# Performance work log

Measured on AMD Instinct MI355X. Metric: run time of the kernel, lower is better.

## Reference

```python
import jax, jax.numpy as jnp
import numpy as np

B, L = 8, 512
D_MODEL, N_HEAD, N_GLOBAL, N_ITER = 64, 8, 64, 4
DAMP_H = 0.0; DAMP_Z = 0.0; STEP_H = 1.0; STEP_Z = 1.0; REG_H = 1.0; REG_Z = 1.0
NEG = -1e9; BIG = 1e9


def sin_pe(length, d):
    # standard additive sinusoidal positional encoding (AddPositionalEncoding)
    pos = np.arange(length, dtype=np.float32)[:, None]
    div = np.exp(np.arange(0, d, 2, dtype=np.float32) * (-np.log(10000.0) / d))
    pe = np.zeros((length, d), dtype=np.float32)
    pe[:, 0::2] = np.sin(pos * div)
    pe[:, 1::2] = np.cos(pos * div)
    return jnp.asarray(pe)


def setup_inputs() -> dict:
    key = jax.random.key(0)
    k1, k2, k3 = jax.random.split(key, 3)
    x = jax.random.normal(k1, (B, L, D_MODEL), jnp.float32)
    mask = jnp.ones((B, L), jnp.int32)
    ternary = jax.random.normal(k2, (D_MODEL, D_MODEL, N_HEAD), jnp.float32)  # std=1 init
    global_w = jax.random.normal(k3, (N_GLOBAL, D_MODEL, 1), jnp.float32) / np.sqrt(D_MODEL)
    return {"x": x, "mask": mask, "ternary": ternary, "global_w": global_w}


def _forward(x, mask, ternary, global_w):
    Bq, Lq, d = x.shape
    norm = lambda a: jax.nn.softmax(a, axis=-1)
    valid = (mask != 0)
    m1 = valid[:, :, None].astype(x.dtype)                      # (B,L,1) keep-mask
    pair = valid[:, None, :, None] & valid[:, None, None, :]    # (B,1,L,L)
    eye_big = BIG * jnp.eye(Lq, dtype=x.dtype)[None, None]      # kill self-edges

    x = x + sin_pe(Lq, d)[None]
    unary = x * m1
    q_z = unary
    q_h1 = jnp.where(pair, 1.0 - eye_big, NEG)                  # (B,H,L,L) via broadcast
    q_h1 = jnp.broadcast_to(q_h1, (Bq, N_HEAD, Lq, Lq))
    q_h2 = jnp.ones((Bq, 1, Lq, N_GLOBAL), x.dtype)             # single-channel: 1 global head

    cache_qh1, cache_qh2 = q_h1, q_h2
    cache_norm_qz = norm(q_z)
    cache_norm_qh1 = norm(q_h1)
    cache_norm_qh2 = norm(q_h2)

    for it in range(N_ITER):
        cache_qz = q_z
        nz = norm(q_z)
        qzn = nz if it == 0 else (1 - STEP_Z) * cache_norm_qz + STEP_Z * nz
        cache_norm_qz = qzn
        qz = qzn * m1
        # F1[z,c,i,j] = sum_{a,b} qz[z,i,a] qz[z,j,b] T[a,b,c]
        t1 = jnp.einsum('zia,abc->zibc', qz, ternary)
        F1 = jnp.einsum('zibc,zjb->zcij', t1, qz)
        F2 = jnp.einsum('zia,jac->zcij', qz, global_w)          # (B,1,L,n_global)
        q_h1 = cache_qh1 * DAMP_H + F1 * (1 - DAMP_H)
        q_h2 = cache_qh2 * DAMP_H + F2 * (1 - DAMP_H)
        cache_qh1, cache_qh2 = q_h1, q_h2
        q_h1m = jnp.where(pair, q_h1 - eye_big, NEG)
        nh1 = norm(q_h1m / REG_H)
        nh2 = norm(q_h2 / REG_H)
        qh1n = nh1 if it == 0 else (1 - STEP_H) * cache_norm_qh1 + STEP_H * nh1
        qh2n = nh2 if it == 0 else (1 - STEP_H) * cache_norm_qh2 + STEP_H * nh2
        cache_norm_qh1, cache_norm_qh2 = qh1n, qh2n
        # messages back to Z: factor (H_i=c, Z_i=a, Z_j=b)
        mi = jnp.einsum('zcij,zjb->zicb', qh1n, qz)
        Mi = jnp.einsum('zicb,abc->zia', mi, ternary)           # to Z_i
        mj = jnp.einsum('zcij,zia->zjca', qh1n, qz)
        Mj = jnp.einsum('zjca,abc->zjb', mj, ternary)           # to Z_j (block_msg=False)
        Mg = jnp.einsum('zcij,jac->zia', qh2n, global_w)        # global-node message
        new_qz = (unary + (Mi + Mj + Mg) / REG_Z) * m1
        q_z = cache_qz * DAMP_Z + new_qz * (1 - DAMP_Z)
    return q_z  # output_prob=False -> unnormalized scores (B,L,d_model)


def reference(x, mask, ternary, global_w):
    return _forward(x, mask, ternary, global_w)
```

## Files before the change

### kernel.cpp

```cpp
#include <hip/hip_runtime.h>

#define BB 8
#define LL 512
#define HH 8
#define BIGV (1e9f)

typedef unsigned short u16;
typedef __attribute__((ext_vector_type(8))) short bf16x8;
typedef __attribute__((ext_vector_type(4))) short s16x4;
typedef __attribute__((ext_vector_type(4))) float f32x4;

#define MFMA(a,b,c) __builtin_amdgcn_mfma_f32_16x16x32_bf16(a,b,c,0,0,0)

__device__ __forceinline__ u16 f2b(float f){
  unsigned u = __float_as_uint(f);
  u = (u + 0x7fffu + ((u>>16)&1u)) >> 16;
  return (u16)u;
}
__device__ __forceinline__ float b2f(u16 s){ return __uint_as_float(((unsigned)s)<<16); }
__device__ __forceinline__ bf16x8 ldb8(const u16* p){ return *(const bf16x8*)p; }

__device__ __forceinline__ float g16_sum(float v){
  v += __shfl_xor(v,1,64); v += __shfl_xor(v,2,64);
  v += __shfl_xor(v,4,64); v += __shfl_xor(v,8,64);
  return v;
}

__global__ void kp_prep(const float* __restrict__ T, const float* __restrict__ gw,
                        u16* __restrict__ T4t, u16* __restrict__ Tt2,
                        u16* __restrict__ Gt, u16* __restrict__ Gt2){
  int idx = blockIdx.x*256 + threadIdx.x;
  { int c=idx>>12, b=(idx>>6)&63, a=idx&63; T4t[idx] = f2b(T[(a*64+b)*8+c]); }
  { int c=idx>>12, a=(idx>>6)&63, b=idx&63; Tt2[idx] = f2b(T[(a*64+b)*8+c]); }
  if(idx < 4096){
    int a=idx>>6, j=idx&63;
    Gt[idx]  = f2b(gw[j*64+a]);
    Gt2[idx] = f2b(gw[idx]);
  }
}

__global__ __launch_bounds__(256) void kCA(const float* __restrict__ x, const int* __restrict__ mask,
      const u16* __restrict__ miP, const u16* __restrict__ mjP, const float* __restrict__ MgF_in,
      float* __restrict__ unary, float* __restrict__ mf,
      const u16* __restrict__ Gt2, const u16* __restrict__ Gt,
      u16* __restrict__ qzb, float* __restrict__ MgF_out, float* __restrict__ out, int mode){
  __shared__ u16 qlds[16*72];
  __shared__ u16 P2s[16*72];
  __shared__ float red2[16*4];
  int bid = blockIdx.x; int z = bid & 7, itile = bid >> 3;
  int t = threadIdx.x, lane = t&63, w = t>>6, l15 = lane&15, lhi = lane>>4;
  int rbase = z*LL + itile*16;
  {
    int row16 = t>>4, c4 = t&15;
    int rg = rbase + row16;
    float v[4]; float mk;
    if(mode == 0){
      mk = (mask[rg] != 0) ? 1.f : 0.f;
      if(c4 == 0) mf[rg] = mk;
      int pos = rg & (LL-1);
      #pragma unroll
      for(int k=0;k<4;k++){
        int d = c4*4 + k;
        float div = __expf(-(float)(d & ~1) * 0.14391156962f);
        float arg = (float)pos * div;
        float pe = (d & 1) ? cosf(arg) : sinf(arg);
        v[k] = (x[(size_t)rg*64 + d] + pe) * mk;
      }
      *(f32x4*)&unary[(size_t)rg*64 + c4*4] = (f32x4){v[0],v[1],v[2],v[3]};
    } else {
      mk = mf[rg];
      f32x4 acc = *(const f32x4*)&MgF_in[(size_t)rg*64 + c4*4];
      #pragma unroll
      for(int c=0;c<8;c++){
        s16x4 vv = *(const s16x4*)&miP[(size_t)rg*512 + c*64 + c4*4];
        acc[0]+=b2f((u16)vv[0]); acc[1]+=b2f((u16)vv[1]);
        acc[2]+=b2f((u16)vv[2]); acc[3]+=b2f((u16)vv[3]);
      }
      #pragma unroll
      for(int s=0;s<4;s++)
        #pragma unroll
        for(int c=0;c<8;c++){
          s16x4 vv = *(const s16x4*)&mjP[(((size_t)(s*8+z))*LL + itile*16 + row16)*512 + c*64 + c4*4];
          acc[0]+=b2f((u16)vv[0]); acc[1]+=b2f((u16)vv[1]);
          acc[2]+=b2f((u16)vv[2]); acc[3]+=b2f((u16)vv[3]);
        }
      f32x4 u0 = *(const f32x4*)&unary[(size_t)rg*64 + c4*4];
      #pragma unroll
      for(int k=0;k<4;k++) v[k] = (u0[k] + acc[k]) * mk;
    }
    if(mode == 2){
      *(f32x4*)&out[(size_t)rg*64 + c4*4] = (f32x4){v[0],v[1],v[2],v[3]};
      return;
    }
    float mx = fmaxf(fmaxf(v[0],v[1]), fmaxf(v[2],v[3]));
    mx = fmaxf(mx, __shfl_xor(mx,1,64));
    mx = fmaxf(mx, __shfl_xor(mx,2,64));
    mx = fmaxf(mx, __shfl_xor(mx,4,64));
    mx = fmaxf(mx, __shfl_xor(mx,8,64));
    float s = 0.f;
    #pragma unroll
    for(int k=0;k<4;k++){ v[k] = __expf(v[k]-mx); s += v[k]; }
    s += __shfl_xor(s,1,64); s += __shfl_xor(s,2,64);
    s += __shfl_xor(s,4,64); s += __shfl_xor(s,8,64);
    float iv = mk / s;
    s16x4 q4 = { (short)f2b(v[0]*iv), (short)f2b(v[1]*iv),
                 (short)f2b(v[2]*iv), (short)f2b(v[3]*iv) };
    *(s16x4*)&qzb[(size_t)rg*64 + c4*4] = q4;
    *(s16x4*)&qlds[row16*72 + c4*4] = q4;
  }
  __syncthreads();
  float fv[4];
  {
    bf16x8 a0 = ldb8(&qlds[l15*72 + lhi*8]);
    bf16x8 a1 = ldb8(&qlds[l15*72 + lhi*8 + 32]);
    const u16* Br = Gt2 + (size_t)(w*16 + l15)*64 + lhi*8;
    f32x4 acc = {0.f,0.f,0.f,0.f};
    acc = MFMA(a0, ldb8(Br), acc);
    acc = MFMA(a1, ldb8(Br+32), acc);
    #pragma unroll
    for(int jj=0;jj<4;jj++){
      float e = __expf(acc[jj]);
      fv[jj] = e;
      float p = g16_sum(e);
      if(l15==0) red2[(lhi*4+jj)*4 + w] = p;
    }
  }
  __syncthreads();
  #pragma unroll
  for(int jj=0;jj<4;jj++){
    int r = lhi*4+jj;
    float s = red2[r*4+0]+red2[r*4+1]+red2[r*4+2]+red2[r*4+3];
    float iv = 1.f/s;
    P2s[r*72 + w*16 + l15] = f2b(fv[jj]*iv);
  }
  __syncthreads();
  {
    bf16x8 a0 = ldb8(&P2s[l15*72 + lhi*8]);
    bf16x8 a1 = ldb8(&P2s[l15*72 + lhi*8 + 32]);
    const u16* Br = Gt + (size_t)(w*16 + l15)*64 + lhi*8;
    f32x4 acc = {0.f,0.f,0.f,0.f};
    acc = MFMA(a0, ldb8(Br), acc);
    acc = MFMA(a1, ldb8(Br+32), acc);
    #pragma unroll
    for(int jj=0;jj<4;jj++)
      MgF_out[((size_t)rbase + lhi*4 + jj)*64 + w*16 + l15] = acc[jj];
  }
}

__global__ __launch_bounds__(256) void k2(const u16* __restrict__ qzb,
      const u16* __restrict__ T4t, const u16* __restrict__ Tt2,
      u16* __restrict__ t1b, u16* __restrict__ t1t, u16* __restrict__ t2t){
  __shared__ u16 s1[64*72];
  __shared__ u16 s2[64*72];
  __shared__ u16 s3[64*72];
  int bid = blockIdx.x; int z = bid&7, c = (bid>>3)&7, itile = bid>>6;
  int zc = z*8 + c;
  int t = threadIdx.x, lane = t&63, w = t>>6, l15 = lane&15, lhi = lane>>4;
  int i0 = itile*64;
  const u16* qA = qzb + ((size_t)z*LL + i0 + w*16 + l15)*64 + lhi*8;
  bf16x8 qa0 = ldb8(qA), qa1 = ldb8(qA+32);
  const u16* tA = T4t + c*4096 + (w*16 + l15)*64 + lhi*8;
  bf16x8 ta0 = ldb8(tA), ta1 = ldb8(tA+32);
  const u16* uA = Tt2 + c*4096 + (w*16 + l15)*64 + lhi*8;
  bf16x8 ua0 = ldb8(uA), ua1 = ldb8(uA+32);
  #pragma unroll
  for(int nt=0;nt<4;nt++){
    {
      const u16* Br = T4t + c*4096 + (nt*16 + l15)*64 + lhi*8;
      f32x4 acc = {0.f,0.f,0.f,0.f};
      acc = MFMA(qa0, ldb8(Br), acc);
      acc = MFMA(qa1, ldb8(Br+32), acc);
      #pragma unroll
      for(int jj=0;jj<4;jj++)
        s1[(w*16 + lhi*4 + jj)*72 + nt*16 + l15] = f2b(acc[jj]);
    }
    const u16* Br = qzb + ((size_t)z*LL + i0 + nt*16 + l15)*64 + lhi*8;
    bf16x8 qb0 = ldb8(Br), qb1 = ldb8(Br+32);
    {
      f32x4 acc = {0.f,0.f,0.f,0.f};
      acc = MFMA(ta0, qb0, acc);
      acc = MFMA(ta1, qb1, acc);
      #pragma unroll
      for(int jj=0;jj<4;jj++)
        s2[(w*16 + lhi*4 + jj)*72 + nt*16 + l15] = f2b(acc[jj]);
    }
    {
      f32x4 acc = {0.f,0.f,0.f,0.f};
      acc = MFMA(ua0, qb0, acc);
      acc = MFMA(ua1, qb1, acc);
      #pragma unroll
      for(int jj=0;jj<4;jj++)
        s3[(w*16 + lhi*4 + jj)*72 + nt*16 + l15] = f2b(acc[jj]);
    }
  }
  __syncthreads();
  #pragma unroll
  for(int p=0;p<2;p++){
    int r = p*32 + (t>>3), ch = t&7;
    *(bf16x8*)&t1b[((size_t)zc*LL + i0 + r)*64 + ch*8]   = *(const bf16x8*)&s1[r*72 + ch*8];
    *(bf16x8*)&t1t[((size_t)zc*64 + r)*LL + i0 + ch*8]   = *(const bf16x8*)&s2[r*72 + ch*8];
    *(bf16x8*)&t2t[((size_t)zc*64 + r)*LL + i0 + ch*8]   = *(const bf16x8*)&s3[r*72 + ch*8];
  }
}

__global__ __launch_bounds__(1024) void kF(const u16* __restrict__ t1b, const u16* __restrict__ qzb,
        const u16* __restrict__ t1t, const u16* __restrict__ t2t, const float* __restrict__ mf,
        u16* __restrict__ miP, u16* __restrict__ mjP){
  extern __shared__ char smem[];
  u16*   t2s  = (u16*)smem;
  u16*   Pp   = (u16*)(smem + 66560);
  u16*   PpT  = (u16*)(smem + 99840);
  float* redS2= (float*)(smem + 140800);
  float* stgf = (float*)(smem + 141056);
  u16*   stg  = (u16*)smem;
  int bid = blockIdx.x;
  int z = bid&7, c = (bid>>3)&7, it = bid>>6;
  int zc = z*8 + c;
  int t = threadIdx.x, lane = t&63, w = t>>6, l15 = lane&15, lhi = lane>>4;
  int jc0 = w*32;
  int h = w>>3, wr = (w>>2)&1, wc = w&3;
  if(t < 64) redS2[t] = 0.f;
  __syncthreads();
  #pragma unroll
  for(int m=0;m<4;m++){
    int e = (m*1024 + t)*8;
    int a = e >> 9, j = e & 511;
    *(bf16x8*)&t2s[a*520 + j] = ldb8(t2t + ((size_t)zc*64 + a)*LL + j);
  }
  float mfj[2];
  mfj[0] = mf[z*LL + jc0 + l15];
  mfj[1] = mf[z*LL + jc0 + 16 + l15];
  f32x4 mj[2][4];
  #pragma unroll
  for(int jt=0;jt<2;jt++)
    #pragma unroll
    for(int bt=0;bt<4;bt++) mj[jt][bt] = (f32x4){0.f,0.f,0.f,0.f};
  u16* PpTw = PpT + w*32*40;

  for(int ip=0; ip<4; ++ip){
    int i0g = it*128 + ip*32;
    int par = ip & 1;
    f32x4 S[2][2];
    #pragma unroll
    for(int rt=0;rt<2;rt++){ S[rt][0] = (f32x4){0,0,0,0}; S[rt][1] = (f32x4){0,0,0,0}; }
    #pragma unroll
    for(int rt=0;rt<2;rt++){
      const u16* Ar = t1b + ((size_t)zc*LL + i0g + rt*16 + l15)*64 + lhi*8;
      bf16x8 a0 = ldb8(Ar), a1 = ldb8(Ar+32);
      #pragma unroll
      for(int ct=0;ct<2;ct++){
        const u16* Br = qzb + ((size_t)z*LL + jc0 + ct*16 + l15)*64 + lhi*8;
        S[rt][ct] = MFMA(a0, ldb8(Br), S[rt][ct]);
        S[rt][ct] = MFMA(a1, ldb8(Br+32), S[rt][ct]);
      }
    }
    #pragma unroll
    for(int rt=0;rt<2;rt++)
      #pragma unroll
      for(int jj=0;jj<4;jj++){
        int rloc = rt*16 + lhi*4 + jj;
        int irow = i0g + rloc;
        float mfi = mf[z*LL + irow];
        float ps = 0.f;
        #pragma unroll
        for(int ct=0;ct<2;ct++){
          int jcol = jc0 + ct*16 + l15;
          float v = S[rt][ct][jj] - ((irow==jcol)?BIGV:0.f);
          float e = mfi * mfj[ct] * __expf(v);
          S[rt][ct][jj] = e; ps += e;
          Pp[rloc*520 + jcol] = f2b(e);
        }
        ps = g16_sum(ps);
        if(l15 == 0) atomicAdd(&redS2[par*32 + rloc], ps);
      }
    __syncthreads();
    if(t < 32) redS2[(par^1)*32 + t] = 0.f;
    float ivv[2][4];
    #pragma unroll
    for(int rt=0;rt<2;rt++)
      #pragma unroll
      for(int jj=0;jj<4;jj++){
        float s = redS2[par*32 + rt*16 + lhi*4 + jj];
        ivv[rt][jj] = s > 0.f ? 1.f/s : 0.f;
      }
    #pragma unroll
    for(int rt=0;rt<2;rt++)
      #pragma unroll
      for(int ct=0;ct<2;ct++){
        s16x4 v4 = { (short)f2b(S[rt][ct][0]*ivv[rt][0]), (short)f2b(S[rt][ct][1]*ivv[rt][1]),
                     (short)f2b(S[rt][ct][2]*ivv[rt][2]), (short)f2b(S[rt][ct][3]*ivv[rt][3]) };
        *(s16x4*)&PpTw[(ct*16 + l15)*40 + rt*16 + lhi*4] = v4;
      }
    {
      f32x4 mia = {0.f,0.f,0.f,0.f};
      const u16* Ab = Pp + (wr*16 + l15)*520 + h*256 + lhi*8;
      const u16* Bb = t2s + (wc*16 + l15)*520 + h*256 + lhi*8;
      #pragma unroll
      for(int ks=0;ks<8;ks++)
        mia = MFMA(ldb8(Ab + ks*32), ldb8(Bb + ks*32), mia);
      #pragma unroll
      for(int jj=0;jj<4;jj++)
        stgf[(h*32 + wr*16 + lhi*4 + jj)*68 + wc*16 + l15] = mia[jj]*ivv[wr][jj];
    }
    {
      bf16x8 av[2];
      #pragma unroll
      for(int jt=0;jt<2;jt++)
        av[jt] = ldb8(PpTw + (jt*16 + l15)*40 + lhi*8);
      #pragma unroll
      for(int bt=0;bt<4;bt++){
        bf16x8 b = ldb8(t1t + ((size_t)zc*64 + bt*16 + l15)*LL + i0g + lhi*8);
        #pragma unroll
        for(int jt=0;jt<2;jt++) mj[jt][bt] = MFMA(av[jt], b, mj[jt][bt]);
      }
    }
    __syncthreads();
    if(t < 512){
      int r = t>>4, cc = t&15;
      f32x4 v0 = *(const f32x4*)&stgf[r*68 + cc*4];
      f32x4 v1 = *(const f32x4*)&stgf[(32+r)*68 + cc*4];
      s16x4 o = { (short)f2b(v0[0]+v1[0]), (short)f2b(v0[1]+v1[1]),
                  (short)f2b(v0[2]+v1[2]), (short)f2b(v0[3]+v1[3]) };
      *(s16x4*)&miP[((size_t)z*LL + i0g + r)*512 + c*64 + cc*4] = o;
    }
  }
  #pragma unroll
  for(int jt=0;jt<2;jt++)
    #pragma unroll
    for(int bt=0;bt<4;bt++)
      #pragma unroll
      for(int jj=0;jj<4;jj++)
        stg[(jc0 + jt*16 + lhi*4 + jj)*72 + bt*16 + l15] = f2b(mj[jt][bt][jj]);
  __syncthreads();
  #pragma unroll
  for(int q=0;q<4;q++){
    int e = q*1024 + t;
    int j = e >> 3, ch = e & 7;
    *(bf16x8*)&mjP[(((size_t)(it*8 + z))*LL + j)*512 + c*64 + ch*8]
      = *(const bf16x8*)&stg[j*72 + ch*8];
  }
}

extern "C" void kernel_launch(void* const* d_in, const int* in_sizes, int n_in,
                              void* d_out, int out_size, void* d_ws, size_t ws_size,
                              hipStream_t stream) {
  const float* x       = (const float*)d_in[0];
  const int*   mask    = (const int*)d_in[1];
  const float* ternary = (const float*)d_in[2];
  const float* gw      = (const float*)d_in[3];
  float* out = (float*)d_out;

  const size_t NE = (size_t)BB*LL*64;
  char* p = (char*)d_ws;
  auto alloc = [&](size_t bytes)->void*{
    void* r = (void*)p; p += (bytes + 255) & ~(size_t)255; return r;
  };
  float* unary   = (float*)alloc(NE*4);
  float* mf      = (float*)alloc((size_t)BB*LL*4);
  u16*   qzb     = (u16*)alloc(NE*2);
  u16*   t1b     = (u16*)alloc((size_t)BB*HH*LL*64*2);
  u16*   t1t     = (u16*)alloc((size_t)BB*HH*LL*64*2);
  u16*   t2t     = (u16*)alloc((size_t)BB*HH*LL*64*2);
  float* MgF     = (float*)alloc(NE*4);
  u16*   miP     = (u16*)alloc((size_t)BB*LL*512*2);
  u16*   mjP     = (u16*)alloc((size_t)32*LL*512*2);
  u16*   T4t     = (u16*)alloc(32768*2);
  u16*   Tt2     = (u16*)alloc(32768*2);
  u16*   Gt      = (u16*)alloc(4096*2);
  u16*   Gt2     = (u16*)alloc(4096*2);

  const int KF_LDS = 158464;
  hipFuncSetAttribute(reinterpret_cast<const void*>(kF),
                      hipFuncAttributeMaxDynamicSharedMemorySize, KF_LDS);

  kp_prep<<<128, 256, 0, stream>>>(ternary, gw, T4t, Tt2, Gt, Gt2);
  kCA<<<256, 256, 0, stream>>>(x, mask, miP, mjP, MgF, unary, mf, Gt2, Gt,
                               qzb, MgF, out, 0);
  for(int it=0; it<4; ++it){
    k2<<<512, 256, 0, stream>>>(qzb, T4t, Tt2, t1b, t1t, t2t);
    kF<<<256, 1024, KF_LDS, stream>>>(t1b, qzb, t1t, t2t, mf, miP, mjP);
    kCA<<<256, 256, 0, stream>>>(x, mask, miP, mjP, MgF, unary, mf, Gt2, Gt,
                                 qzb, MgF, out, (it==3) ? 2 : 1);
  }
}
```

Before: 220.3 us.

## Split kF blocks by j-half to double grid and halve LDS per block

After: 310.7 us. +41.1%, slower.

```diff
diff --git a/kernel.cpp b/kernel.cpp
--- a/kernel.cpp
+++ b/kernel.cpp
@@ -40,7 +40,7 @@
 }
 
 __global__ __launch_bounds__(256) void kCA(const float* __restrict__ x, const int* __restrict__ mask,
-      const u16* __restrict__ miP, const u16* __restrict__ mjP, const float* __restrict__ MgF_in,
+      const u16* __restrict__ miP2, const u16* __restrict__ mjP, const float* __restrict__ MgF_in,
       float* __restrict__ unary, float* __restrict__ mf,
       const u16* __restrict__ Gt2, const u16* __restrict__ Gt,
       u16* __restrict__ qzb, float* __restrict__ MgF_out, float* __restrict__ out, int mode){
@@ -53,6 +53,7 @@
   {
     int row16 = t>>4, c4 = t&15;
     int rg = rbase + row16;
+    int rloc = itile*16 + row16;
     float v[4]; float mk;
     if(mode == 0){
       mk = (mask[rg] != 0) ? 1.f : 0.f;
@@ -71,16 +72,18 @@
       mk = mf[rg];
       f32x4 acc = *(const f32x4*)&MgF_in[(size_t)rg*64 + c4*4];
       #pragma unroll
-      for(int c=0;c<8;c++){
-        s16x4 vv = *(const s16x4*)&miP[(size_t)rg*512 + c*64 + c4*4];
-        acc[0]+=b2f((u16)vv[0]); acc[1]+=b2f((u16)vv[1]);
-        acc[2]+=b2f((u16)vv[2]); acc[3]+=b2f((u16)vv[3]);
-      }
+      for(int hh=0;hh<2;hh++)
+        #pragma unroll
+        for(int c=0;c<8;c++){
+          s16x4 vv = *(const s16x4*)&miP2[(((size_t)(hh*8+z))*LL + rloc)*512 + c*64 + c4*4];
+          acc[0]+=b2f((u16)vv[0]); acc[1]+=b2f((u16)vv[1]);
+          acc[2]+=b2f((u16)vv[2]); acc[3]+=b2f((u16)vv[3]);
+        }
       #pragma unroll
       for(int s=0;s<4;s++)
         #pragma unroll
         for(int c=0;c<8;c++){
-          s16x4 vv = *(const s16x4*)&mjP[(((size_t)(s*8+z))*LL + itile*16 + row16)*512 + c*64 + c4*4];
+          s16x4 vv = *(const s16x4*)&mjP[(((size_t)(s*8+z))*LL + rloc)*512 + c*64 + c4*4];
           acc[0]+=b2f((u16)vv[0]); acc[1]+=b2f((u16)vv[1]);
           acc[2]+=b2f((u16)vv[2]); acc[3]+=b2f((u16)vv[3]);
         }
@@ -205,27 +208,29 @@
 
 __global__ __launch_bounds__(1024) void kF(const u16* __restrict__ t1b, const u16* __restrict__ qzb,
         const u16* __restrict__ t1t, const u16* __restrict__ t2t, const float* __restrict__ mf,
-        u16* __restrict__ miP, u16* __restrict__ mjP){
+        u16* __restrict__ miP2, u16* __restrict__ mjP){
   extern __shared__ char smem[];
-  u16*   t2s  = (u16*)smem;
-  u16*   Pp   = (u16*)(smem + 66560);
-  u16*   PpT  = (u16*)(smem + 99840);
-  float* redS2= (float*)(smem + 140800);
-  float* stgf = (float*)(smem + 141056);
+  u16*   t2sh = (u16*)smem;
+  u16*   Pph  = (u16*)(smem + 33792);
+  u16*   PpT  = (u16*)(smem + 50688);
+  float* redS2= (float*)(smem + 71168);
+  float* stgf = (float*)(smem + 71424);
   u16*   stg  = (u16*)smem;
   int bid = blockIdx.x;
-  int z = bid&7, c = (bid>>3)&7, it = bid>>6;
+  int z = bid&7, c = (bid>>3)&7, it = (bid>>6)&3, h = bid>>8;
   int zc = z*8 + c;
   int t = threadIdx.x, lane = t&63, w = t>>6, l15 = lane&15, lhi = lane>>4;
   int jc0 = w*32;
-  int h = w>>3, wr = (w>>2)&1, wc = w&3;
+  int inh = ((w>>3) == h);
+  int win = w & 7;
+  int wr2 = (win>>2)&1, wc2 = win&3;
   if(t < 64) redS2[t] = 0.f;
   __syncthreads();
   #pragma unroll
-  for(int m=0;m<4;m++){
+  for(int m=0;m<2;m++){
     int e = (m*1024 + t)*8;
-    int a = e >> 9, j = e & 511;
-    *(bf16x8*)&t2s[a*520 + j] = ldb8(t2t + ((size_t)zc*64 + a)*LL + j);
+    int a = e >> 8, j = e & 255;
+    *(bf16x8*)&t2sh[a*264 + j] = ldb8(t2t + ((size_t)zc*64 + a)*LL + h*256 + j);
   }
   float mfj[2];
   mfj[0] = mf[z*LL + jc0 + l15];
@@ -235,7 +240,7 @@
   for(int jt=0;jt<2;jt++)
     #pragma unroll
     for(int bt=0;bt<4;bt++) mj[jt][bt] = (f32x4){0.f,0.f,0.f,0.f};
-  u16* PpTw = PpT + w*32*40;
+  u16* PpTw = PpT + win*32*40;
 
   for(int ip=0; ip<4; ++ip){
     int i0g = it*128 + ip*32;
@@ -268,7 +273,7 @@
           float v = S[rt][ct][jj] - ((irow==jcol)?BIGV:0.f);
           float e = mfi * mfj[ct] * __expf(v);
           S[rt][ct][jj] = e; ps += e;
-          Pp[rloc*520 + jcol] = f2b(e);
+          if(inh) Pph[rloc*264 + win*32 + ct*16 + l15] = f2b(e);
         }
         ps = g16_sum(ps);
         if(l15 == 0) atomicAdd(&redS2[par*32 + rloc], ps);
@@ -283,60 +288,60 @@
         float s = redS2[par*32 + rt*16 + lhi*4 + jj];
         ivv[rt][jj] = s > 0.f ? 1.f/s : 0.f;
       }
-    #pragma unroll
-    for(int rt=0;rt<2;rt++)
-      #pragma unroll
-      for(int ct=0;ct<2;ct++){
-        s16x4 v4 = { (short)f2b(S[rt][ct][0]*ivv[rt][0]), (short)f2b(S[rt][ct][1]*ivv[rt][1]),
-                     (short)f2b(S[rt][ct][2]*ivv[rt][2]), (short)f2b(S[rt][ct][3]*ivv[rt][3]) };
-        *(s16x4*)&PpTw[(ct*16 + l15)*40 + rt*16 + lhi*4] = v4;
-      }
-    {
+    if(inh){
+      #pragma unroll
+      for(int rt=0;rt<2;rt++)
+        #pragma unroll
+        for(int ct=0;ct<2;ct++){
+          s16x4 v4 = { (short)f2b(S[rt][ct][0]*ivv[rt][0]), (short)f2b(S[rt][ct][1]*ivv[rt][1]),
+                       (short)f2b(S[rt][ct][2]*ivv[rt][2]), (short)f2b(S[rt][ct][3]*ivv[rt][3]) };
+          *(s16x4*)&PpTw[(ct*16 + l15)*40 + rt*16 + lhi*4] = v4;
+        }
+      bf16x8 av[2];
+      #pragma unroll
+      for(int jt=0;jt<2;jt++)
+        av[jt] = ldb8(PpTw + (jt*16 + l15)*40 + lhi*8);
+      #pragma unroll
+      for(int bt=0;bt<4;bt++){
+        bf16x8 b = ldb8(t1t + ((size_t)zc*64 + bt*16 + l15)*LL + i0g + lhi*8);
+        #pragma unroll
+        for(int jt=0;jt<2;jt++) mj[jt][bt] = MFMA(av[jt], b, mj[jt][bt]);
+      }
+    } else {
       f32x4 mia = {0.f,0.f,0.f,0.f};
-      const u16* Ab = Pp + (wr*16 + l15)*520 + h*256 + lhi*8;
-      const u16* Bb = t2s + (wc*16 + l15)*520 + h*256 + lhi*8;
+      const u16* Ab = Pph + (wr2*16 + l15)*264 + lhi*8;
+      const u16* Bb = t2sh + (wc2*16 + l15)*264 + lhi*8;
       #pragma unroll
       for(int ks=0;ks<8;ks++)
         mia = MFMA(ldb8(Ab + ks*32), ldb8(Bb + ks*32), mia);
       #pragma unroll
       for(int jj=0;jj<4;jj++)
-        stgf[(h*32 + wr*16 + lhi*4 + jj)*68 + wc*16 + l15] = mia[jj]*ivv[wr][jj];
-    }
-    {
-      bf16x8 av[2];
-      #pragma unroll
-      for(int jt=0;jt<2;jt++)
-        av[jt] = ldb8(PpTw + (jt*16 + l15)*40 + lhi*8);
-      #pragma unroll
-      for(int bt=0;bt<4;bt++){
-        bf16x8 b = ldb8(t1t + ((size_t)zc*64 + bt*16 + l15)*LL + i0g + lhi*8);
-        #pragma unroll
-        for(int jt=0;jt<2;jt++) mj[jt][bt] = MFMA(av[jt], b, mj[jt][bt]);
-      }
+        stgf[(wr2*16 + lhi*4 + jj)*68 + wc2*16 + l15] = mia[jj]*ivv[wr2][jj];
     }
     __syncthreads();
     if(t < 512){
       int r = t>>4, cc = t&15;
       f32x4 v0 = *(const f32x4*)&stgf[r*68 + cc*4];
-      f32x4 v1 = *(const f32x4*)&stgf[(32+r)*68 + cc*4];
-      s16x4 o = { (short)f2b(v0[0]+v1[0]), (short)f2b(v0[1]+v1[1]),
-                  (short)f2b(v0[2]+v1[2]), (short)f2b(v0[3]+v1[3]) };
-      *(s16x4*)&miP[((size_t)z*LL + i0g + r)*512 + c*64 + cc*4] = o;
-    }
-  }
-  #pragma unroll
-  for(int jt=0;jt<2;jt++)
-    #pragma unroll
-    for(int bt=0;bt<4;bt++)
-      #pragma unroll
-      for(int jj=0;jj<4;jj++)
-        stg[(jc0 + jt*16 + lhi*4 + jj)*72 + bt*16 + l15] = f2b(mj[jt][bt][jj]);
-  __syncthreads();
-  #pragma unroll
-  for(int q=0;q<4;q++){
+      s16x4 o = { (short)f2b(v0[0]), (short)f2b(v0[1]),
+                  (short)f2b(v0[2]), (short)f2b(v0[3]) };
+      *(s16x4*)&miP2[(((size_t)(h*8 + z))*LL + i0g + r)*512 + c*64 + cc*4] = o;
+    }
+  }
+  if(inh){
+    #pragma unroll
+    for(int jt=0;jt<2;jt++)
+      #pragma unroll
+      for(int bt=0;bt<4;bt++)
+        #pragma unroll
+        for(int jj=0;jj<4;jj++)
+          stg[(win*32 + jt*16 + lhi*4 + jj)*72 + bt*16 + l15] = f2b(mj[jt][bt][jj]);
+  }
+  __syncthreads();
+  #pragma unroll
+  for(int q=0;q<2;q++){
     int e = q*1024 + t;
     int j = e >> 3, ch = e & 7;
-    *(bf16x8*)&mjP[(((size_t)(it*8 + z))*LL + j)*512 + c*64 + ch*8]
+    *(bf16x8*)&mjP[(((size_t)(it*8 + z))*LL + h*256 + j)*512 + c*64 + ch*8]
       = *(const bf16x8*)&stg[j*72 + ch*8];
   }
 }
@@ -362,24 +367,24 @@
   u16*   t1t     = (u16*)alloc((size_t)BB*HH*LL*64*2);
   u16*   t2t     = (u16*)alloc((size_t)BB*HH*LL*64*2);
   float* MgF     = (float*)alloc(NE*4);
-  u16*   miP     = (u16*)alloc((size_t)BB*LL*512*2);
+  u16*   miP2    = (u16*)alloc((size_t)2*BB*LL*512*2);
   u16*   mjP     = (u16*)alloc((size_t)32*LL*512*2);
   u16*   T4t     = (u16*)alloc(32768*2);
   u16*   Tt2     = (u16*)alloc(32768*2);
   u16*   Gt      = (u16*)alloc(4096*2);
   u16*   Gt2     = (u16*)alloc(4096*2);
 
-  const int KF_LDS = 158464;
+  const int KF_LDS = 80128;
   hipFuncSetAttribute(reinterpret_cast<const void*>(kF),
                       hipFuncAttributeMaxDynamicSharedMemorySize, KF_LDS);
 
   kp_prep<<<128, 256, 0, stream>>>(ternary, gw, T4t, Tt2, Gt, Gt2);
-  kCA<<<256, 256, 0, stream>>>(x, mask, miP, mjP, MgF, unary, mf, Gt2, Gt,
+  kCA<<<256, 256, 0, stream>>>(x, mask, miP2, mjP, MgF, unary, mf, Gt2, Gt,
                                qzb, MgF, out, 0);
   for(int it=0; it<4; ++it){
     k2<<<512, 256, 0, stream>>>(qzb, T4t, Tt2, t1b, t1t, t2t);
-    kF<<<256, 1024, KF_LDS, stream>>>(t1b, qzb, t1t, t2t, mf, miP, mjP);
-    kCA<<<256, 256, 0, stream>>>(x, mask, miP, mjP, MgF, unary, mf, Gt2, Gt,
+    kF<<<512, 1024, KF_LDS, stream>>>(t1b, qzb, t1t, t2t, mf, miP2, mjP);
+    kCA<<<256, 256, 0, stream>>>(x, mask, miP2, mjP, MgF, unary, mf, Gt2, Gt,
                                  qzb, MgF, out, (it==3) ? 2 : 1);
   }
 }
```
